# Performance work log

Measured on AMD Instinct MI355X. Metric: run time of the kernel, lower is better.

## Reference

```python
import jax, jax.numpy as jnp
import numpy as np

F_DIM, HID, H, DQ, DV = 1024, 4096, 16, 64, 64
EPS = 1e-6

def layer_norm(x, w, b):
    mu = jnp.mean(x, axis=-1, keepdims=True)
    var = jnp.mean(jnp.square(x - mu), axis=-1, keepdims=True)
    return (x - mu) * jax.lax.rsqrt(var + EPS) * w + b

def setup_inputs() -> dict:
    key = jax.random.key(0)
    ks = jax.random.split(key, 8)
    s = 0.02
    return {
        'x': jax.random.normal(ks[0], (4, 2048, F_DIM), dtype=jnp.float32),
        'ln1_w': jnp.ones((F_DIM,), jnp.float32),
        'ln1_b': jnp.zeros((F_DIM,), jnp.float32),
        'wq_w': jax.random.normal(ks[1], (H * DQ, F_DIM), jnp.float32) * s,
        'wq_b': jnp.zeros((H * DQ,), jnp.float32),
        'wk_w': jax.random.normal(ks[2], (H * DQ, F_DIM), jnp.float32) * s,
        'wk_b': jnp.zeros((H * DQ,), jnp.float32),
        'wv_w': jax.random.normal(ks[3], (H * DV, F_DIM), jnp.float32) * s,
        'wv_b': jnp.zeros((H * DV,), jnp.float32),
        'fc_w': jax.random.normal(ks[4], (F_DIM, H * DV), jnp.float32) * s,
        'fc_b': jnp.zeros((F_DIM,), jnp.float32),
        'ln2_w': jnp.ones((F_DIM,), jnp.float32),
        'ln2_b': jnp.zeros((F_DIM,), jnp.float32),
        'fc1_w': jax.random.normal(ks[5], (HID, F_DIM), jnp.float32) * s,
        'fc1_b': jnp.zeros((HID,), jnp.float32),
        'fc2_w': jax.random.normal(ks[6], (F_DIM, HID), jnp.float32) * s,
        'fc2_b': jnp.zeros((F_DIM,), jnp.float32),
    }

def reference(x, ln1_w, ln1_b, wq_w, wq_b, wk_w, wk_b, wv_w, wv_b,
              fc_w, fc_b, ln2_w, ln2_b, fc1_w, fc1_b, fc2_w, fc2_b):
    B, S, _ = x.shape
    # --- pre-LN multi-head self-attention ---
    h = layer_norm(x, ln1_w, ln1_b)
    q = (h @ wq_w.T + wq_b).reshape(B, S, H, DQ).transpose(0, 2, 1, 3)  # [B,H,S,dq]
    k = (h @ wk_w.T + wk_b).reshape(B, S, H, DQ).transpose(0, 2, 1, 3)
    v = (h @ wv_w.T + wv_b).reshape(B, S, H, DV).transpose(0, 2, 1, 3)
    attn = jax.nn.softmax(jnp.einsum('bhqd,bhkd->bhqk', q, k) / jnp.sqrt(jnp.float32(DQ)), axis=-1)
    out = jnp.einsum('bhqk,bhkd->bhqd', attn, v).transpose(0, 2, 1, 3).reshape(B, S, H * DV)
    x = x + (out @ fc_w.T + fc_b)
    # --- pre-LN residual MLP ---
    h2 = layer_norm(x, ln2_w, ln2_b)
    ff = jax.nn.relu(h2 @ fc1_w.T + fc1_b) @ fc2_w.T + fc2_b
    return x + ff
```

## Files before the change

### kernel.cpp

```cpp
#include <hip/hip_runtime.h>

#define F_DIMC 1024
#define HIDC   4096
#define NH     16
#define SEQ    2048
#define BATCH  4
#define ROWS   (BATCH * SEQ)
#define MEG    (1u << 20)
#define QSCALE 0.18033688011112042f

typedef unsigned short u16t;
typedef __attribute__((ext_vector_type(8))) short short8;
typedef __attribute__((ext_vector_type(4))) float floatx4;
typedef __attribute__((address_space(1))) void gvoid_t;
typedef __attribute__((address_space(3))) void lvoid_t;
#define ASYNC16(g, l) __builtin_amdgcn_global_load_lds((gvoid_t*)(g), (lvoid_t*)(l), 16, 0, 0)

#if __has_builtin(__builtin_amdgcn_exp2f)
#define EXP2(x) __builtin_amdgcn_exp2f(x)
#else
#define EXP2(x) exp2f(x)
#endif

__device__ __forceinline__ u16t f2bf(float f) {
    union { float f; unsigned u; } v; v.f = f;
    unsigned r = v.u + 0x7fffu + ((v.u >> 16) & 1u);
    return (u16t)(r >> 16);
}
__device__ __forceinline__ unsigned fasu(float f) {
    union { float f; unsigned u; } v; v.f = f; return v.u;
}

__global__ __launch_bounds__(256) void ln_kernel(const float* __restrict__ x,
                                                 const float* __restrict__ w,
                                                 const float* __restrict__ b,
                                                 u16t* __restrict__ out) {
    const int row = blockIdx.x;
    const int t = threadIdx.x;
    const float* xp = x + (size_t)row * F_DIMC;

    float4 v = *(const float4*)(xp + t * 4);
    float s  = v.x + v.y + v.z + v.w;
    float ss = v.x * v.x + v.y * v.y + v.z * v.z + v.w * v.w;
    for (int off = 32; off; off >>= 1) {
        s  += __shfl_down(s, off);
        ss += __shfl_down(ss, off);
    }
    __shared__ float red[8];
    const int wid = t >> 6, lid = t & 63;
    if (lid == 0) { red[wid] = s; red[4 + wid] = ss; }
    __syncthreads();
    if (t == 0) {
        float S  = red[0] + red[1] + red[2] + red[3];
        float SS = red[4] + red[5] + red[6] + red[7];
        float mu  = S * (1.0f / F_DIMC);
        float var = SS * (1.0f / F_DIMC) - mu * mu;
        red[0] = mu;
        red[1] = rsqrtf(var + 1e-6f);
    }
    __syncthreads();
    const float mu = red[0], rs = red[1];

    float4 wv = *(const float4*)(w + t * 4);
    float4 bv = *(const float4*)(b + t * 4);
    ushort4 o = make_ushort4(f2bf((v.x - mu) * rs * wv.x + bv.x),
                             f2bf((v.y - mu) * rs * wv.y + bv.y),
                             f2bf((v.z - mu) * rs * wv.z + bv.z),
                             f2bf((v.w - mu) * rs * wv.w + bv.w));
    *(ushort4*)(out + (size_t)row * F_DIMC + t * 4) = o;
}

__global__ __launch_bounds__(256) void wconv_kernel(const float* __restrict__ w0,
        const float* __restrict__ w1, const float* __restrict__ w2,
        const float* __restrict__ w3, const float* __restrict__ w4,
        const float* __restrict__ w5, u16t* __restrict__ dst) {
    const size_t e = ((size_t)blockIdx.x * 256 + threadIdx.x) * 4;
    const float* src; size_t off;
    if      (e < 1 * MEG) { src = w0; off = e; }
    else if (e < 2 * MEG) { src = w1; off = e - 1 * MEG; }
    else if (e < 3 * MEG) { src = w2; off = e - 2 * MEG; }
    else if (e < 4 * MEG) { src = w3; off = e - 3 * MEG; }
    else if (e < 8 * MEG) { src = w4; off = e - 4 * MEG; }
    else                  { src = w5; off = e - 8 * MEG; }
    float4 f = *(const float4*)(src + off);
    *(ushort4*)(dst + e) = make_ushort4(f2bf(f.x), f2bf(f.y), f2bf(f.z), f2bf(f.w));
}

#define GEMM_PROLOGUE_AND_LOOP(Aq, Wq, Kdim)                                   \
    __shared__ u16t As[128 * 32] __attribute__((aligned(16)));                 \
    __shared__ u16t Ws[128 * 32] __attribute__((aligned(16)));                 \
    const int t = threadIdx.x;                                                 \
    const int lane = t & 63;                                                   \
    const int wave = t >> 6;                                                   \
    const int wm = wave >> 1, wn = wave & 1;                                   \
    const int m0 = blockIdx.y * 128, n0 = blockIdx.x * 128;                    \
    const int b0 = t, b1 = t + 256;                                            \
    const int r0 = b0 >> 2, r1 = b1 >> 2;                                      \
    const int q0_ = (b0 & 3) ^ (r0 & 3) ^ ((r0 >> 2) & 1);                     \
    const int q1_ = (b1 & 3) ^ (r1 & 3) ^ ((r1 >> 2) & 1);                     \
    const u16t* Ag0 = (Aq) + (size_t)(m0 + r0) * (Kdim) + q0_ * 8;             \
    const u16t* Ag1 = (Aq) + (size_t)(m0 + r1) * (Kdim) + q1_ * 8;             \
    const u16t* Wg0 = (Wq) + (size_t)(n0 + r0) * (Kdim) + q0_ * 8;             \
    const u16t* Wg1 = (Wq) + (size_t)(n0 + r1) * (Kdim) + q1_ * 8;             \
    u16t* Al0 = As + b0 * 8;  u16t* Al1 = As + b1 * 8;                         \
    u16t* Wl0 = Ws + b0 * 8;  u16t* Wl1 = Ws + b1 * 8;                         \
    const int fm = lane & 15, fq = lane >> 4;                                  \
    const int swz = fq ^ (fm & 3) ^ ((fm >> 2) & 1);                           \
    const u16t* Afp = As + ((wm * 64 + fm) * 32 + swz * 8);                    \
    const u16t* Wfp = Ws + ((wn * 64 + fm) * 32 + swz * 8);                    \
    floatx4 acc[4][4] = {};                                                    \
    for (int k0 = 0; k0 < (Kdim); k0 += 32) {                                  \
        ASYNC16(Ag0, Al0); ASYNC16(Ag1, Al1);                                  \
        ASYNC16(Wg0, Wl0); ASYNC16(Wg1, Wl1);                                  \
        Ag0 += 32; Ag1 += 32; Wg0 += 32; Wg1 += 32;                            \
        __syncthreads();                                                       \
        short8 fa[4], fb[4];                                                   \
        _Pragma("unroll")                                                      \
        for (int i = 0; i < 4; ++i) {                                          \
            fa[i] = *(const short8*)(Afp + i * 16 * 32);                       \
            fb[i] = *(const short8*)(Wfp + i * 16 * 32);                       \
        }                                                                      \
        _Pragma("unroll")                                                      \
        for (int mi = 0; mi < 4; ++mi)                                         \
            _Pragma("unroll")                                                  \
            for (int ni = 0; ni < 4; ++ni)                                     \
                acc[mi][ni] = __builtin_amdgcn_mfma_f32_16x16x32_bf16(         \
                    fa[mi], fb[ni], acc[mi][ni], 0, 0, 0);                     \
        __syncthreads();                                                       \
    }

template <bool RELU, bool RES, bool BF16OUT>
__global__ __launch_bounds__(256) void gemm_mfma(const u16t* __restrict__ A,
                                                 const u16t* __restrict__ W,
                                                 const float* __restrict__ bias,
                                                 const float* res, void* Cout,
                                                 int N, int K) {
    GEMM_PROLOGUE_AND_LOOP(A, W, K)
    float bl[4];
#pragma unroll
    for (int ni = 0; ni < 4; ++ni) bl[ni] = bias[n0 + wn * 64 + ni * 16 + fm];
#pragma unroll
    for (int mi = 0; mi < 4; ++mi) {
#pragma unroll
        for (int ni = 0; ni < 4; ++ni) {
            const int col = n0 + wn * 64 + ni * 16 + fm;
#pragma unroll
            for (int r = 0; r < 4; ++r) {
                const int row = m0 + wm * 64 + mi * 16 + fq * 4 + r;
                const size_t off = (size_t)row * N + col;
                float c = acc[mi][ni][r] + bl[ni];
                if (RELU) c = fmaxf(c, 0.0f);
                if (RES)  c += res[off];
                if (BF16OUT) ((u16t*)Cout)[off] = f2bf(c);
                else         ((float*)Cout)[off] = c;
            }
        }
    }
}

__global__ __launch_bounds__(256) void gemm_qkv(const u16t* __restrict__ A,
        const u16t* __restrict__ W,
        const float* __restrict__ wq_b, const float* __restrict__ wk_b,
        const float* __restrict__ wv_b,
        u16t* __restrict__ qb, u16t* __restrict__ kb, u16t* __restrict__ vtb) {
    GEMM_PROLOGUE_AND_LOOP(A, W, F_DIMC)
    const int which = n0 >> 10;
    const int nb = n0 & 1023;
    const float* bias = which == 0 ? wq_b : which == 1 ? wk_b : wv_b;
    float bl[4];
#pragma unroll
    for (int ni = 0; ni < 4; ++ni) bl[ni] = bias[nb + wn * 64 + ni * 16 + fm];

    if (which == 2) {
#pragma unroll
        for (int mi = 0; mi < 4; ++mi)
#pragma unroll
            for (int ni = 0; ni < 4; ++ni) {
                const int col = nb + wn * 64 + ni * 16 + fm;
                const int row0 = m0 + wm * 64 + mi * 16 + fq * 4;
                ushort4 pk = make_ushort4(f2bf(acc[mi][ni][0] + bl[ni]),
                                          f2bf(acc[mi][ni][1] + bl[ni]),
                                          f2bf(acc[mi][ni][2] + bl[ni]),
                                          f2bf(acc[mi][ni][3] + bl[ni]));
                *(ushort4*)(vtb + (size_t)col * ROWS + row0) = pk;
            }
    } else {
        u16t* dst = (which == 0) ? qb : kb;
        const float sc = (which == 0) ? QSCALE : 1.0f;
#pragma unroll
        for (int mi = 0; mi < 4; ++mi)
#pragma unroll
            for (int ni = 0; ni < 4; ++ni) {
                const int col = nb + wn * 64 + ni * 16 + fm;
#pragma unroll
                for (int r = 0; r < 4; ++r) {
                    const int row = m0 + wm * 64 + mi * 16 + fq * 4 + r;
                    dst[(size_t)row * F_DIMC + col] = f2bf((acc[mi][ni][r] + bl[ni]) * sc);
                }
            }
    }
}

__global__ __launch_bounds__(256, 4) void attn_mfma(const u16t* __restrict__ qb,
        const u16t* __restrict__ kbuf, const u16t* __restrict__ vtb,
        u16t* __restrict__ ab) {
    __shared__ u16t Kt[2][64 * 64] __attribute__((aligned(16)));
    __shared__ u16t Vs[64 * 64] __attribute__((aligned(16)));
    __shared__ u16t QP[128 * 64] __attribute__((aligned(16)));

    const int t = threadIdx.x;
    const int lane = t & 63;
    const int wave = t >> 6;
    const int l15 = lane & 15, q4 = lane >> 4;
    const int q0 = blockIdx.x * 128;
    const int bh = blockIdx.y;
    const int b = bh >> 4, hh = bh & 15;

#pragma unroll
    for (int c = 0; c < 4; ++c) {
        const int beta = c * 256 + t;
        const int r = beta >> 3, o = (beta & 7) ^ (r & 7);
        ASYNC16(qb + (size_t)(b * SEQ + q0 + r) * F_DIMC + hh * 64 + o * 8,
                QP + beta * 8);
    }
    const u16t* kg = kbuf + (size_t)(b * SEQ) * F_DIMC + hh * 64;
    const u16t* vg = vtb + (size_t)(hh * 64) * ROWS + b * SEQ;

    const int sb0 = t, sb1 = t + 256;
    const int sr0 = sb0 >> 3, so0 = (sb0 & 7) ^ (sr0 & 7);
    const int sr1 = sb1 >> 3, so1 = (sb1 & 7) ^ (sr1 & 7);
    const u16t* kp0 = kg + (size_t)sr0 * F_DIMC + so0 * 8;
    const u16t* kp1 = kg + (size_t)sr1 * F_DIMC + so1 * 8;
    const u16t* vp0 = vg + (size_t)sr0 * ROWS + so0 * 8;
    const u16t* vp1 = vg + (size_t)sr1 * ROWS + so1 * 8;

    ASYNC16(kp0, Kt[0] + sb0 * 8);
    ASYNC16(kp1, Kt[0] + sb1 * 8);
    ASYNC16(vp0, Vs + sb0 * 8);
    ASYNC16(vp1, Vs + sb1 * 8);
    kp0 += 64 * F_DIMC; kp1 += 64 * F_DIMC; vp0 += 64; vp1 += 64;
    __syncthreads();

    short8 fqr[2][2];
#pragma unroll
    for (int mt = 0; mt < 2; ++mt)
#pragma unroll
        for (int ks = 0; ks < 2; ++ks) {
            const int m = wave * 32 + mt * 16 + l15;
            const int oct = ks * 4 + q4;
            fqr[mt][ks] = *(const short8*)(QP + (m * 8 + (oct ^ (m & 7))) * 8);
        }

    short8 ones;
#pragma unroll
    for (int i = 0; i < 8; ++i) ones[i] = (short)0x3F80;

    floatx4 oacc[2][4] = {};
    floatx4 lacc[2] = {};

    for (int it = 0; it < SEQ / 64; ++it) {
        if (it + 1 < SEQ / 64) {
            u16t* kd = Kt[(it + 1) & 1];
            ASYNC16(kp0, kd + sb0 * 8);
            ASYNC16(kp1, kd + sb1 * 8);
            kp0 += 64 * F_DIMC; kp1 += 64 * F_DIMC;
        }
        const u16t* kcur = Kt[it & 1];

        short8 fk[4][2];
#pragma unroll
        for (int nt = 0; nt < 4; ++nt)
#pragma unroll
            for (int ks = 0; ks < 2; ++ks) {
                const int kr = nt * 16 + l15;
                const int oct = ks * 4 + q4;
                fk[nt][ks] = *(const short8*)(kcur + (kr * 8 + (oct ^ (kr & 7))) * 8);
            }
        floatx4 st[2][4] = {};
#pragma unroll
        for (int mt = 0; mt < 2; ++mt)
#pragma unroll
            for (int nt = 0; nt < 4; ++nt) {
                st[mt][nt] = __builtin_amdgcn_mfma_f32_16x16x32_bf16(
                    fk[nt][0], fqr[mt][0], st[mt][nt], 0, 0, 0);
                st[mt][nt] = __builtin_amdgcn_mfma_f32_16x16x32_bf16(
                    fk[nt][1], fqr[mt][1], st[mt][nt], 0, 0, 0);
            }

#pragma unroll
        for (int mt = 0; mt < 2; ++mt)
#pragma unroll
            for (int nt = 0; nt < 4; ++nt) {
                const float p0 = EXP2(st[mt][nt][0]);
                const float p1 = EXP2(st[mt][nt][1]);
                const float p2 = EXP2(st[mt][nt][2]);
                const float p3 = EXP2(st[mt][nt][3]);
                const unsigned lo = __builtin_amdgcn_perm(fasu(p1), fasu(p0), 0x07060302u);
                const unsigned hi = __builtin_amdgcn_perm(fasu(p3), fasu(p2), 0x07060302u);
                const int m = wave * 32 + mt * 16 + l15;
                const int logb = nt * 2 + (q4 >> 1);
                *(uint2*)(QP + (m * 8 + (logb ^ (m & 7))) * 8 + (q4 & 1) * 4) =
                    make_uint2(lo, hi);
            }

        __syncthreads();

        short8 fp[2][2], fv[4][2];
#pragma unroll
        for (int mt = 0; mt < 2; ++mt)
#pragma unroll
            for (int ks = 0; ks < 2; ++ks) {
                const int m = wave * 32 + mt * 16 + l15;
                const int oct = ks * 4 + q4;
                fp[mt][ks] = *(const short8*)(QP + (m * 8 + (oct ^ (m & 7))) * 8);
            }
#pragma unroll
        for (int nd = 0; nd < 4; ++nd)
#pragma unroll
            for (int ks = 0; ks < 2; ++ks) {
                const int d = nd * 16 + l15;
                const int oct = ks * 4 + q4;
                fv[nd][ks] = *(const short8*)(Vs + (d * 8 + (oct ^ (d & 7))) * 8);
            }
#pragma unroll
        for (int mt = 0; mt < 2; ++mt) {
#pragma unroll
            for (int nd = 0; nd < 4; ++nd) {
                oacc[mt][nd] = __builtin_amdgcn_mfma_f32_16x16x32_bf16(
                    fp[mt][0], fv[nd][0], oacc[mt][nd], 0, 0, 0);
                oacc[mt][nd] = __builtin_amdgcn_mfma_f32_16x16x32_bf16(
                    fp[mt][1], fv[nd][1], oacc[mt][nd], 0, 0, 0);
            }
            lacc[mt] = __builtin_amdgcn_mfma_f32_16x16x32_bf16(
                fp[mt][0], ones, lacc[mt], 0, 0, 0);
            lacc[mt] = __builtin_amdgcn_mfma_f32_16x16x32_bf16(
                fp[mt][1], ones, lacc[mt], 0, 0, 0);
        }

        __syncthreads();
        if (it + 1 < SEQ / 64) {
            ASYNC16(vp0, Vs + sb0 * 8);
            ASYNC16(vp1, Vs + sb1 * 8);
            vp0 += 64; vp1 += 64;
        }
    }

#pragma unroll
    for (int mt = 0; mt < 2; ++mt) {
        floatx4 rinv;
#pragma unroll
        for (int r = 0; r < 4; ++r) rinv[r] = 1.0f / lacc[mt][r];
#pragma unroll
        for (int nd = 0; nd < 4; ++nd)
#pragma unroll
            for (int r = 0; r < 4; ++r) {
                const int row = b * SEQ + q0 + wave * 32 + mt * 16 + q4 * 4 + r;
                const int col = hh * 64 + nd * 16 + l15;
                ab[(size_t)row * F_DIMC + col] = f2bf(oacc[mt][nd][r] * rinv[r]);
            }
    }
}

extern "C" void kernel_launch(void* const* d_in, const int* in_sizes, int n_in,
                              void* d_out, int out_size, void* d_ws, size_t ws_size,
                              hipStream_t stream) {
    const float* x     = (const float*)d_in[0];
    const float* ln1_w = (const float*)d_in[1];
    const float* ln1_b = (const float*)d_in[2];
    const float* wq_w  = (const float*)d_in[3];
    const float* wq_b  = (const float*)d_in[4];
    const float* wk_w  = (const float*)d_in[5];
    const float* wk_b  = (const float*)d_in[6];
    const float* wv_w  = (const float*)d_in[7];
    const float* wv_b  = (const float*)d_in[8];
    const float* fc_w  = (const float*)d_in[9];
    const float* fc_b  = (const float*)d_in[10];
    const float* ln2_w = (const float*)d_in[11];
    const float* ln2_b = (const float*)d_in[12];
    const float* fc1_w = (const float*)d_in[13];
    const float* fc1_b = (const float*)d_in[14];
    const float* fc2_w = (const float*)d_in[15];
    const float* fc2_b = (const float*)d_in[16];

    float* out = (float*)d_out;
    u16t*  ws  = (u16t*)d_ws;

    u16t* wbuf = ws;
    u16t* bwqkv = wbuf;
    u16t* bwfc = wbuf + 3 * MEG;
    u16t* bwf1 = wbuf + 4 * MEG;
    u16t* bwf2 = wbuf + 8 * MEG;
    u16t* h    = wbuf + 12 * MEG;
    u16t* qb   = h + 8 * MEG;
    u16t* kb   = qb + 8 * MEG;
    u16t* vtb  = kb + 8 * MEG;
    u16t* ab   = vtb + 8 * MEG;
    u16t* ff   = qb;

    const dim3 blk(256);
    const dim3 gF(F_DIMC / 128, ROWS / 128);
    const dim3 gQKV(3072 / 128, ROWS / 128);
    const dim3 gH(HIDC / 128, ROWS / 128);

    wconv_kernel<<<12 * MEG / 1024, blk, 0, stream>>>(wq_w, wk_w, wv_w, fc_w, fc1_w, fc2_w, wbuf);
    ln_kernel<<<ROWS, blk, 0, stream>>>(x, ln1_w, ln1_b, h);
    gemm_qkv<<<gQKV, blk, 0, stream>>>(h, bwqkv, wq_b, wk_b, wv_b, qb, kb, vtb);
    attn_mfma<<<dim3(SEQ / 128, BATCH * NH), blk, 0, stream>>>(qb, kb, vtb, ab);
    gemm_mfma<false, true, false><<<gF, blk, 0, stream>>>(ab, bwfc, fc_b, x, out, F_DIMC, F_DIMC);
    ln_kernel<<<ROWS, blk, 0, stream>>>(out, ln2_w, ln2_b, h);
    gemm_mfma<true, false, true><<<gH, blk, 0, stream>>>(h, bwf1, fc1_b, nullptr, ff, HIDC, F_DIMC);
    gemm_mfma<false, true, false><<<gF, blk, 0, stream>>>(ff, bwf2, fc2_b, out, out, F_DIMC, HIDC);
}
```

Measured before the change: 575.4 us.

## Double-buffer GEMM with 256x128 tiles, K=64 steps and XCD-aware block swizzle

Replaces the single-buffered 128x128, K=32 GEMM main loop with a 512-thread, 256x128-tile kernel. It double-buffers K=64 slices in LDS using async global-to-LDS loads, so fetching the next tile overlaps the MFMA work on the current one. It also adds an XOR LDS swizzle for 64-wide rows, s_setprio around MFMA bursts, and a 1D grid remapped so neighbouring tiles land on the same XCD for better L2 reuse. The cost is higher LDS use (about 96KB per block), which limits occupancy, plus hand-placed waitcnt and barrier logic that must stay correct.

```diff
diff --git a/kernel.cpp b/kernel.cpp
--- a/kernel.cpp
+++ b/kernel.cpp
@@ -86,56 +86,127 @@
     *(ushort4*)(dst + e) = make_ushort4(f2bf(f.x), f2bf(f.y), f2bf(f.z), f2bf(f.w));
 }
 
-#define GEMM_PROLOGUE_AND_LOOP(Aq, Wq, Kdim)                                   \
-    __shared__ u16t As[128 * 32] __attribute__((aligned(16)));                 \
-    __shared__ u16t Ws[128 * 32] __attribute__((aligned(16)));                 \
+#define DP_PROLOGUE_AND_LOOP(Aq, Wq, Kdim, NBX)                                \
+    __shared__ u16t As[2][256 * 64] __attribute__((aligned(16)));              \
+    __shared__ u16t Ws[2][128 * 64] __attribute__((aligned(16)));              \
     const int t = threadIdx.x;                                                 \
     const int lane = t & 63;                                                   \
     const int wave = t >> 6;                                                   \
     const int wm = wave >> 1, wn = wave & 1;                                   \
-    const int m0 = blockIdx.y * 128, n0 = blockIdx.x * 128;                    \
-    const int b0 = t, b1 = t + 256;                                            \
-    const int r0 = b0 >> 2, r1 = b1 >> 2;                                      \
-    const int q0_ = (b0 & 3) ^ (r0 & 3) ^ ((r0 >> 2) & 1);                     \
-    const int q1_ = (b1 & 3) ^ (r1 & 3) ^ ((r1 >> 2) & 1);                     \
-    const u16t* Ag0 = (Aq) + (size_t)(m0 + r0) * (Kdim) + q0_ * 8;             \
-    const u16t* Ag1 = (Aq) + (size_t)(m0 + r1) * (Kdim) + q1_ * 8;             \
-    const u16t* Wg0 = (Wq) + (size_t)(n0 + r0) * (Kdim) + q0_ * 8;             \
-    const u16t* Wg1 = (Wq) + (size_t)(n0 + r1) * (Kdim) + q1_ * 8;             \
-    u16t* Al0 = As + b0 * 8;  u16t* Al1 = As + b1 * 8;                         \
-    u16t* Wl0 = Ws + b0 * 8;  u16t* Wl1 = Ws + b1 * 8;                         \
     const int fm = lane & 15, fq = lane >> 4;                                  \
-    const int swz = fq ^ (fm & 3) ^ ((fm >> 2) & 1);                           \
-    const u16t* Afp = As + ((wm * 64 + fm) * 32 + swz * 8);                    \
-    const u16t* Wfp = Ws + ((wn * 64 + fm) * 32 + swz * 8);                    \
+    const int l7 = lane & 7;                                                   \
+         \
+    const int nwg = gridDim.x;                                                 \
+    const int swzb = (blockIdx.x & 7) * (nwg >> 3) + (blockIdx.x >> 3);        \
+    const int m0 = (swzb / (NBX)) * 256, n0 = (swzb % (NBX)) * 128;            \
+               \
+    const u16t* ag[4]; const u16t* wg2[2];                                     \
+    int alo[4]; int wlo[2];                                                    \
+    _Pragma("unroll")                                                          \
+    for (int i = 0; i < 4; ++i) {                                              \
+        const int beta = i * 512 + t;                                          \
+        const int r = beta >> 3, j = (beta & 7) ^ (r & 7);                     \
+        ag[i] = (Aq) + (size_t)(m0 + r) * (Kdim) + j * 8;                      \
+        alo[i] = beta * 8;                                                     \
+    }                                                                          \
+    _Pragma("unroll")                                                          \
+    for (int i = 0; i < 2; ++i) {                                              \
+        const int beta = i * 512 + t;                                          \
+        const int r = beta >> 3, j = (beta & 7) ^ (r & 7);                     \
+        wg2[i] = (Wq) + (size_t)(n0 + r) * (Kdim) + j * 8;                     \
+        wlo[i] = beta * 8;                                                     \
+    }                                                                          \
+          \
+    int abase[2], bbase[2];                                                    \
+    _Pragma("unroll")                                                          \
+    for (int ks = 0; ks < 2; ++ks) {                                           \
+        const int sw = (ks * 4 + fq) ^ l7;                                     \
+        abase[ks] = (wm * 64 + fm) * 64 + sw * 8;                              \
+        bbase[ks] = (wn * 64 + fm) * 64 + sw * 8;                              \
+    }                                                                          \
+    const int NT = (Kdim) / 64;                                                \
+                       \
+    _Pragma("unroll")                                                          \
+    for (int i = 0; i < 4; ++i) ASYNC16(ag[i], &As[0][alo[i]]);                \
+    _Pragma("unroll")                                                          \
+    for (int i = 0; i < 2; ++i) ASYNC16(wg2[i], &Ws[0][wlo[i]]);               \
+    _Pragma("unroll")                                                          \
+    for (int i = 0; i < 4; ++i) ASYNC16(ag[i] + 64, &As[1][alo[i]]);           \
+    _Pragma("unroll")                                                          \
+    for (int i = 0; i < 2; ++i) ASYNC16(wg2[i] + 64, &Ws[1][wlo[i]]);          \
+    _Pragma("unroll")                                                          \
+    for (int i = 0; i < 4; ++i) ag[i] += 128;                                  \
+    _Pragma("unroll")                                                          \
+    for (int i = 0; i < 2; ++i) wg2[i] += 128;                                 \
+    asm volatile("s_waitcnt vmcnt(6)" ::: "memory");         \
+    __builtin_amdgcn_s_barrier();                                              \
+    __builtin_amdgcn_sched_barrier(0);                                         \
     floatx4 acc[4][4] = {};                                                    \
-    for (int k0 = 0; k0 < (Kdim); k0 += 32) {                                  \
-        ASYNC16(Ag0, Al0); ASYNC16(Ag1, Al1);                                  \
-        ASYNC16(Wg0, Wl0); ASYNC16(Wg1, Wl1);                                  \
-        Ag0 += 32; Ag1 += 32; Wg0 += 32; Wg1 += 32;                            \
-        __syncthreads();                                                       \
+    for (int tt = 0; tt < NT; ++tt) {                                          \
+        const u16t* Ab = As[tt & 1];                                           \
+        const u16t* Wb = Ws[tt & 1];                                           \
+                                      \
         short8 fa[4], fb[4];                                                   \
         _Pragma("unroll")                                                      \
-        for (int i = 0; i < 4; ++i) {                                          \
-            fa[i] = *(const short8*)(Afp + i * 16 * 32);                       \
-            fb[i] = *(const short8*)(Wfp + i * 16 * 32);                       \
-        }                                                                      \
+        for (int mi = 0; mi < 4; ++mi)                                         \
+            fa[mi] = *(const short8*)(Ab + abase[0] + mi * 1024);              \
+        _Pragma("unroll")                                                      \
+        for (int ni = 0; ni < 4; ++ni)                                         \
+            fb[ni] = *(const short8*)(Wb + bbase[0] + ni * 1024);              \
+        __builtin_amdgcn_s_setprio(1);                                         \
         _Pragma("unroll")                                                      \
         for (int mi = 0; mi < 4; ++mi)                                         \
             _Pragma("unroll")                                                  \
             for (int ni = 0; ni < 4; ++ni)                                     \
                 acc[mi][ni] = __builtin_amdgcn_mfma_f32_16x16x32_bf16(         \
                     fa[mi], fb[ni], acc[mi][ni], 0, 0, 0);                     \
-        __syncthreads();                                                       \
+        __builtin_amdgcn_s_setprio(0);                                         \
+                     \
+        short8 fa1[4], fb1[4];                                                 \
+        _Pragma("unroll")                                                      \
+        for (int mi = 0; mi < 4; ++mi)                                         \
+            fa1[mi] = *(const short8*)(Ab + abase[1] + mi * 1024);             \
+        _Pragma("unroll")                                                      \
+        for (int ni = 0; ni < 4; ++ni)                                         \
+            fb1[ni] = *(const short8*)(Wb + bbase[1] + ni * 1024);             \
+        asm volatile("s_waitcnt lgkmcnt(0)" ::: "memory");  \
+        __builtin_amdgcn_s_barrier();        \
+        __builtin_amdgcn_sched_barrier(0);                                     \
+        if (tt + 2 < NT) {                                                     \
+            const int pb = tt & 1;           \
+            _Pragma("unroll")                                                  \
+            for (int i = 0; i < 4; ++i) {                                      \
+                ASYNC16(ag[i], &As[pb][alo[i]]); ag[i] += 64;                  \
+            }                                                                  \
+            _Pragma("unroll")                                                  \
+            for (int i = 0; i < 2; ++i) {                                      \
+                ASYNC16(wg2[i], &Ws[pb][wlo[i]]); wg2[i] += 64;                \
+            }                                                                  \
+                  \
+            asm volatile("s_waitcnt vmcnt(6)" ::: "memory");                   \
+        } else {                                                               \
+            asm volatile("s_waitcnt vmcnt(0)" ::: "memory");                   \
+        }                                                                      \
+        __builtin_amdgcn_s_barrier();                                          \
+        __builtin_amdgcn_sched_barrier(0);                                     \
+              \
+        __builtin_amdgcn_s_setprio(1);                                         \
+        _Pragma("unroll")                                                      \
+        for (int mi = 0; mi < 4; ++mi)                                         \
+            _Pragma("unroll")                                                  \
+            for (int ni = 0; ni < 4; ++ni)                                     \
+                acc[mi][ni] = __builtin_amdgcn_mfma_f32_16x16x32_bf16(         \
+                    fa1[mi], fb1[ni], acc[mi][ni], 0, 0, 0);                   \
+        __builtin_amdgcn_s_setprio(0);                                         \
     }
 
 template <bool RELU, bool RES, bool BF16OUT>
-__global__ __launch_bounds__(256) void gemm_mfma(const u16t* __restrict__ A,
-                                                 const u16t* __restrict__ W,
-                                                 const float* __restrict__ bias,
-                                                 const float* res, void* Cout,
-                                                 int N, int K) {
-    GEMM_PROLOGUE_AND_LOOP(A, W, K)
+__global__ __launch_bounds__(512, 2) void gemm_dp(const u16t* __restrict__ A,
+                                                  const u16t* __restrict__ W,
+                                                  const float* __restrict__ bias,
+                                                  const float* res, void* Cout,
+                                                  int N, int K) {
+    DP_PROLOGUE_AND_LOOP(A, W, K, N / 128)
     float bl[4];
 #pragma unroll
     for (int ni = 0; ni < 4; ++ni) bl[ni] = bias[n0 + wn * 64 + ni * 16 + fm];
@@ -158,12 +229,12 @@
     }
 }
 
-__global__ __launch_bounds__(256) void gemm_qkv(const u16t* __restrict__ A,
+__global__ __launch_bounds__(512, 2) void gemm_qkv(const u16t* __restrict__ A,
         const u16t* __restrict__ W,
         const float* __restrict__ wq_b, const float* __restrict__ wk_b,
         const float* __restrict__ wv_b,
         u16t* __restrict__ qb, u16t* __restrict__ kb, u16t* __restrict__ vtb) {
-    GEMM_PROLOGUE_AND_LOOP(A, W, F_DIMC)
+    DP_PROLOGUE_AND_LOOP(A, W, F_DIMC, 3072 / 128)
     const int which = n0 >> 10;
     const int nb = n0 & 1023;
     const float* bias = which == 0 ? wq_b : which == 1 ? wk_b : wv_b;
@@ -398,16 +469,17 @@
     u16t* ff   = qb;
 
     const dim3 blk(256);
-    const dim3 gF(F_DIMC / 128, ROWS / 128);
-    const dim3 gQKV(3072 / 128, ROWS / 128);
-    const dim3 gH(HIDC / 128, ROWS / 128);
+    const dim3 blk512(512);
+    const int gQKV = (ROWS / 256) * (3072 / 128);
+    const int gF   = (ROWS / 256) * (F_DIMC / 128);
+    const int gH   = (ROWS / 256) * (HIDC / 128);
 
     wconv_kernel<<<12 * MEG / 1024, blk, 0, stream>>>(wq_w, wk_w, wv_w, fc_w, fc1_w, fc2_w, wbuf);
     ln_kernel<<<ROWS, blk, 0, stream>>>(x, ln1_w, ln1_b, h);
-    gemm_qkv<<<gQKV, blk, 0, stream>>>(h, bwqkv, wq_b, wk_b, wv_b, qb, kb, vtb);
+    gemm_qkv<<<gQKV, blk512, 0, stream>>>(h, bwqkv, wq_b, wk_b, wv_b, qb, kb, vtb);
     attn_mfma<<<dim3(SEQ / 128, BATCH * NH), blk, 0, stream>>>(qb, kb, vtb, ab);
-    gemm_mfma<false, true, false><<<gF, blk, 0, stream>>>(ab, bwfc, fc_b, x, out, F_DIMC, F_DIMC);
+    gemm_dp<false, true, false><<<gF, blk512, 0, stream>>>(ab, bwfc, fc_b, x, out, F_DIMC, F_DIMC);
     ln_kernel<<<ROWS, blk, 0, stream>>>(out, ln2_w, ln2_b, h);
-    gemm_mfma<true, false, true><<<gH, blk, 0, stream>>>(h, bwf1, fc1_b, nullptr, ff, HIDC, F_DIMC);
-    gemm_mfma<false, true, false><<<gF, blk, 0, stream>>>(ff, bwf2, fc2_b, out, out, F_DIMC, HIDC);
-}
+    gemm_dp<true, false, true><<<gH, blk512, 0, stream>>>(h, bwf1, fc1_b, nullptr, ff, HIDC, F_DIMC);
+    gemm_dp<false, true, false><<<gF, blk512, 0, stream>>>(ff, bwf2, fc2_b, out, out, F_DIMC, HIDC);
+}
```

Measured after the change: 514.7 us. 10.5% less time.

## Double-buffer GEMM LDS tiles with async prefetch and XCD-aware block swizzle

Applied to the files above, without the earlier changes.

Rewrites the shared GEMM core to use two LDS buffers, prefetching the K-tile two steps ahead via global_load_lds. Explicit vmcnt/lgkmcnt waits and raw barriers replace the two __syncthreads per iteration, and s_setprio is raised around the MFMA block. The grid becomes 1D, with blocks remapped in chunks of eight (matching the MI355X's eight XCDs) to improve L2 locality, and launch bounds request 3 waves per SIMD. The LDS swizzle is simplified, which doubles LDS use and may bring back bank conflicts.

```diff
diff --git a/kernel.cpp b/kernel.cpp
--- a/kernel.cpp
+++ b/kernel.cpp
@@ -86,56 +86,79 @@
     *(ushort4*)(dst + e) = make_ushort4(f2bf(f.x), f2bf(f.y), f2bf(f.z), f2bf(f.w));
 }
 
-#define GEMM_PROLOGUE_AND_LOOP(Aq, Wq, Kdim)                                   \
-    __shared__ u16t As[128 * 32] __attribute__((aligned(16)));                 \
-    __shared__ u16t Ws[128 * 32] __attribute__((aligned(16)));                 \
+#define DP_CORE(Aq, Wq, Kdim)                                                  \
+    __shared__ u16t As[2][128 * 32] __attribute__((aligned(16)));              \
+    __shared__ u16t Ws[2][128 * 32] __attribute__((aligned(16)));              \
     const int t = threadIdx.x;                                                 \
     const int lane = t & 63;                                                   \
     const int wave = t >> 6;                                                   \
     const int wm = wave >> 1, wn = wave & 1;                                   \
-    const int m0 = blockIdx.y * 128, n0 = blockIdx.x * 128;                    \
-    const int b0 = t, b1 = t + 256;                                            \
-    const int r0 = b0 >> 2, r1 = b1 >> 2;                                      \
-    const int q0_ = (b0 & 3) ^ (r0 & 3) ^ ((r0 >> 2) & 1);                     \
-    const int q1_ = (b1 & 3) ^ (r1 & 3) ^ ((r1 >> 2) & 1);                     \
-    const u16t* Ag0 = (Aq) + (size_t)(m0 + r0) * (Kdim) + q0_ * 8;             \
-    const u16t* Ag1 = (Aq) + (size_t)(m0 + r1) * (Kdim) + q1_ * 8;             \
-    const u16t* Wg0 = (Wq) + (size_t)(n0 + r0) * (Kdim) + q0_ * 8;             \
-    const u16t* Wg1 = (Wq) + (size_t)(n0 + r1) * (Kdim) + q1_ * 8;             \
-    u16t* Al0 = As + b0 * 8;  u16t* Al1 = As + b1 * 8;                         \
-    u16t* Wl0 = Ws + b0 * 8;  u16t* Wl1 = Ws + b1 * 8;                         \
     const int fm = lane & 15, fq = lane >> 4;                                  \
-    const int swz = fq ^ (fm & 3) ^ ((fm >> 2) & 1);                           \
-    const u16t* Afp = As + ((wm * 64 + fm) * 32 + swz * 8);                    \
-    const u16t* Wfp = Ws + ((wn * 64 + fm) * 32 + swz * 8);                    \
+                           \
+    const int nwg = gridDim.x;                                                 \
+    const int swzb = (blockIdx.x & 7) * (nwg >> 3) + (blockIdx.x >> 3);        \
+    const int m0 = (swzb & 63) * 128;                \
+    const int n0 = (swzb >> 6) * 128;                                          \
+       \
+    const int beta0 = t, beta1 = t + 256;                                      \
+    const int r0 = beta0 >> 2, j0 = (beta0 & 3) ^ (r0 & 3);                    \
+    const int r1 = beta1 >> 2, j1 = (beta1 & 3) ^ (r1 & 3);                    \
+    const u16t* ag0 = (Aq) + (size_t)(m0 + r0) * (Kdim) + j0 * 8;              \
+    const u16t* ag1 = (Aq) + (size_t)(m0 + r1) * (Kdim) + j1 * 8;              \
+    const u16t* wg0 = (Wq) + (size_t)(n0 + r0) * (Kdim) + j0 * 8;              \
+    const u16t* wg1 = (Wq) + (size_t)(n0 + r1) * (Kdim) + j1 * 8;              \
+    const int l0 = beta0 * 8, l1 = beta1 * 8;                                  \
+       \
+    const int aoff = (wm * 64 + fm) * 32 + ((fq ^ (fm & 3)) * 8);              \
+    const int boff = (wn * 64 + fm) * 32 + ((fq ^ (fm & 3)) * 8);              \
+    const int NT = (Kdim) / 32;                                                \
+            \
+    ASYNC16(ag0, &As[0][l0]); ASYNC16(ag1, &As[0][l1]);                        \
+    ASYNC16(wg0, &Ws[0][l0]); ASYNC16(wg1, &Ws[0][l1]);                        \
+    ASYNC16(ag0 + 32, &As[1][l0]); ASYNC16(ag1 + 32, &As[1][l1]);              \
+    ASYNC16(wg0 + 32, &Ws[1][l0]); ASYNC16(wg1 + 32, &Ws[1][l1]);              \
+    ag0 += 64; ag1 += 64; wg0 += 64; wg1 += 64;                                \
+    asm volatile("s_waitcnt vmcnt(4)" ::: "memory");                           \
+    __builtin_amdgcn_s_barrier();                                              \
     floatx4 acc[4][4] = {};                                                    \
-    for (int k0 = 0; k0 < (Kdim); k0 += 32) {                                  \
-        ASYNC16(Ag0, Al0); ASYNC16(Ag1, Al1);                                  \
-        ASYNC16(Wg0, Wl0); ASYNC16(Wg1, Wl1);                                  \
-        Ag0 += 32; Ag1 += 32; Wg0 += 32; Wg1 += 32;                            \
-        __syncthreads();                                                       \
+    for (int tt = 0; tt < NT; ++tt) {                                          \
+        const u16t* Ab = &As[tt & 1][0];                                       \
+        const u16t* Wb = &Ws[tt & 1][0];                                       \
         short8 fa[4], fb[4];                                                   \
         _Pragma("unroll")                                                      \
         for (int i = 0; i < 4; ++i) {                                          \
-            fa[i] = *(const short8*)(Afp + i * 16 * 32);                       \
-            fb[i] = *(const short8*)(Wfp + i * 16 * 32);                       \
+            fa[i] = *(const short8*)(Ab + aoff + i * 512);                     \
+            fb[i] = *(const short8*)(Wb + boff + i * 512);                     \
         }                                                                      \
+        asm volatile("s_waitcnt lgkmcnt(0)" ::: "memory");  \
+        __builtin_amdgcn_s_barrier();               \
+        if (tt + 2 < NT) {                                                     \
+            u16t* la = &As[tt & 1][0]; u16t* lw = &Ws[tt & 1][0];              \
+            ASYNC16(ag0, la + l0); ASYNC16(ag1, la + l1);                      \
+            ASYNC16(wg0, lw + l0); ASYNC16(wg1, lw + l1);                      \
+            ag0 += 32; ag1 += 32; wg0 += 32; wg1 += 32;                        \
+            asm volatile("s_waitcnt vmcnt(4)" ::: "memory");   \
+        } else {                                                               \
+            asm volatile("s_waitcnt vmcnt(0)" ::: "memory");                   \
+        }                                                                      \
+        __builtin_amdgcn_s_barrier();                \
+        __builtin_amdgcn_s_setprio(1);                                         \
         _Pragma("unroll")                                                      \
         for (int mi = 0; mi < 4; ++mi)                                         \
             _Pragma("unroll")                                                  \
             for (int ni = 0; ni < 4; ++ni)                                     \
                 acc[mi][ni] = __builtin_amdgcn_mfma_f32_16x16x32_bf16(         \
                     fa[mi], fb[ni], acc[mi][ni], 0, 0, 0);                     \
-        __syncthreads();                                                       \
+        __builtin_amdgcn_s_setprio(0);                                         \
     }
 
 template <bool RELU, bool RES, bool BF16OUT>
-__global__ __launch_bounds__(256) void gemm_mfma(const u16t* __restrict__ A,
-                                                 const u16t* __restrict__ W,
-                                                 const float* __restrict__ bias,
-                                                 const float* res, void* Cout,
-                                                 int N, int K) {
-    GEMM_PROLOGUE_AND_LOOP(A, W, K)
+__global__ __launch_bounds__(256, 3) void gemm_dp(const u16t* __restrict__ A,
+                                                  const u16t* __restrict__ W,
+                                                  const float* __restrict__ bias,
+                                                  const float* res, void* Cout,
+                                                  int N, int K) {
+    DP_CORE(A, W, K)
     float bl[4];
 #pragma unroll
     for (int ni = 0; ni < 4; ++ni) bl[ni] = bias[n0 + wn * 64 + ni * 16 + fm];
@@ -158,12 +181,12 @@
     }
 }
 
-__global__ __launch_bounds__(256) void gemm_qkv(const u16t* __restrict__ A,
+__global__ __launch_bounds__(256, 3) void gemm_qkv(const u16t* __restrict__ A,
         const u16t* __restrict__ W,
         const float* __restrict__ wq_b, const float* __restrict__ wk_b,
         const float* __restrict__ wv_b,
         u16t* __restrict__ qb, u16t* __restrict__ kb, u16t* __restrict__ vtb) {
-    GEMM_PROLOGUE_AND_LOOP(A, W, F_DIMC)
+    DP_CORE(A, W, F_DIMC)
     const int which = n0 >> 10;
     const int nb = n0 & 1023;
     const float* bias = which == 0 ? wq_b : which == 1 ? wk_b : wv_b;
@@ -186,7 +209,7 @@
             }
     } else {
         u16t* dst = (which == 0) ? qb : kb;
-        const float sc = (which == 0) ? QSCALE : 1.0f;
+        const float sc2 = (which == 0) ? QSCALE : 1.0f;
 #pragma unroll
         for (int mi = 0; mi < 4; ++mi)
 #pragma unroll
@@ -195,7 +218,7 @@
 #pragma unroll
                 for (int r = 0; r < 4; ++r) {
                     const int row = m0 + wm * 64 + mi * 16 + fq * 4 + r;
-                    dst[(size_t)row * F_DIMC + col] = f2bf((acc[mi][ni][r] + bl[ni]) * sc);
+                    dst[(size_t)row * F_DIMC + col] = f2bf((acc[mi][ni][r] + bl[ni]) * sc2);
                 }
             }
     }
@@ -398,16 +421,16 @@
     u16t* ff   = qb;
 
     const dim3 blk(256);
-    const dim3 gF(F_DIMC / 128, ROWS / 128);
-    const dim3 gQKV(3072 / 128, ROWS / 128);
-    const dim3 gH(HIDC / 128, ROWS / 128);
+    const int gQKV = 64 * (3072 / 128);
+    const int gF   = 64 * (F_DIMC / 128);
+    const int gH   = 64 * (HIDC / 128);
 
     wconv_kernel<<<12 * MEG / 1024, blk, 0, stream>>>(wq_w, wk_w, wv_w, fc_w, fc1_w, fc2_w, wbuf);
     ln_kernel<<<ROWS, blk, 0, stream>>>(x, ln1_w, ln1_b, h);
     gemm_qkv<<<gQKV, blk, 0, stream>>>(h, bwqkv, wq_b, wk_b, wv_b, qb, kb, vtb);
     attn_mfma<<<dim3(SEQ / 128, BATCH * NH), blk, 0, stream>>>(qb, kb, vtb, ab);
-    gemm_mfma<false, true, false><<<gF, blk, 0, stream>>>(ab, bwfc, fc_b, x, out, F_DIMC, F_DIMC);
+    gemm_dp<false, true, false><<<gF, blk, 0, stream>>>(ab, bwfc, fc_b, x, out, F_DIMC, F_DIMC);
     ln_kernel<<<ROWS, blk, 0, stream>>>(out, ln2_w, ln2_b, h);
-    gemm_mfma<true, false, true><<<gH, blk, 0, stream>>>(h, bwf1, fc1_b, nullptr, ff, HIDC, F_DIMC);
-    gemm_mfma<false, true, false><<<gF, blk, 0, stream>>>(ff, bwf2, fc2_b, out, out, F_DIMC, HIDC);
-}
+    gemm_dp<true, false, true><<<gH, blk, 0, stream>>>(h, bwf1, fc1_b, nullptr, ff, HIDC, F_DIMC);
+    gemm_dp<false, true, false><<<gF, blk, 0, stream>>>(ff, bwf2, fc2_b, out, out, F_DIMC, HIDC);
+}
```

Result: faster. 553.5 us (-3.8%).
